# Optimization experiments

Hardware: AMD Instinct MI355X
Metric: run time of the kernel (lower is better)

Reference implementation:

```python
import jax, jax.numpy as jnp
import numpy as np

B, S, D, H = 256, 200, 256, 4
HD = D // H
R = 16  # HIE reduced rank (hardcoded in module)
EPS = 1e-12


def setup_inputs() -> dict:
    key = jax.random.key(0)
    ks = jax.random.split(key, 32)
    w = lambda k, sh: jax.random.normal(k, sh, jnp.float32) * 0.02
    inp = {
        'input_tensor': jax.random.normal(ks[0], (B, S, D), jnp.float32),
        'fusion_tensor': jax.random.normal(ks[1], (B, S, D), jnp.float32),
        'pos_tensor': jax.random.normal(ks[2], (B, S, D), jnp.float32),
        'attention_mask': jnp.zeros((B, 1, 1, S), jnp.float32),
        # projections (stored as (in, out); apply as x @ W + b)
        'Wv': w(ks[3], (D, D)), 'bv': w(ks[4], (D,)),
        'Wqf': w(ks[5], (D, D)), 'bqf': w(ks[6], (D,)),
        'Wkf': w(ks[7], (D, D)), 'bkf': w(ks[8], (D,)),
        'Wvf': w(ks[9], (D, D)), 'bvf': w(ks[10], (D,)),
        'Wqp': w(ks[11], (D, D)), 'bqp': w(ks[12], (D,)),
        'Wkp': w(ks[13], (D, D)), 'bkp': w(ks[14], (D,)),
        'Wvp': w(ks[15], (D, D)), 'bvp': w(ks[16], (D,)),
        # output dense + LayerNorm per branch
        'Wd': w(ks[17], (D, D)), 'bd': w(ks[18], (D,)),
        'g1': jnp.ones((D,), jnp.float32), 'b1': jnp.zeros((D,), jnp.float32),
        'Wfd': w(ks[19], (D, D)), 'bfd': w(ks[20], (D,)),
        'g2': jnp.ones((D,), jnp.float32), 'b2': jnp.zeros((D,), jnp.float32),
        'Wpd': w(ks[21], (D, D)), 'bpd': w(ks[22], (D,)),
        'g3': jnp.ones((D,), jnp.float32), 'b3': jnp.zeros((D,), jnp.float32),
        # HIE parameter (n, r)
        'Wr': jax.random.normal(ks[23], (S, R), jnp.float32),
    }
    return inp


def _heads(t):
    # (B,S,D) -> (B,H,S,HD)
    return t.reshape(B, S, H, HD).transpose(0, 2, 1, 3)


def _layernorm(x, g, b):
    m = jnp.mean(x, axis=-1, keepdims=True)
    v = jnp.mean((x - m) ** 2, axis=-1, keepdims=True)
    return (x - m) * jax.lax.rsqrt(v + EPS) * g + b


def _compute(resid, value_layer, scores, mask, Wd, bd, g, b):
    s = scores / np.sqrt(HD) + mask
    probs = jax.nn.softmax(s, axis=-1)  # (attn dropout = identity in eval)
    ctx = jnp.einsum('bhqk,bhkd->bhqd', probs, value_layer)
    ctx = ctx.transpose(0, 2, 1, 3).reshape(B, S, D)
    return _layernorm(ctx @ Wd + bd + resid, g, b)


def _hie(hX, hA, Wr):
    # reduce sequence dim, batched QR on (d, r) columns
    hr = jnp.einsum('bnd,nr->brd', hX, Wr)        # (B,R,D)
    Q, _ = jnp.linalg.qr(hr.transpose(0, 2, 1))   # (B,D,R), reduced
    pX = hX @ Q                                    # (B,S,R)
    pA = hA @ Q
    pAt = (pX * pA > 0).astype(pA.dtype) * pA      # indicator gate
    return jnp.einsum('bnr,bdr->bnd', pAt, Q)


def reference(input_tensor, fusion_tensor, pos_tensor, attention_mask,
              Wv, bv, Wqf, bqf, Wkf, bkf, Wvf, bvf, Wqp, bqp, Wkp, bkp,
              Wvp, bvp, Wd, bd, g1, b1, Wfd, bfd, g2, b2, Wpd, bpd, g3, b3, Wr):
    item_v = _heads(input_tensor @ Wv + bv)
    fq = _heads(fusion_tensor @ Wqf + bqf)
    fk = _heads(fusion_tensor @ Wkf + bkf)
    fv = _heads(fusion_tensor @ Wvf + bvf)
    pq = _heads(pos_tensor @ Wqp + bqp)
    pk = _heads(pos_tensor @ Wkp + bkp)
    pv = _heads(pos_tensor @ Wvp + bvp)

    item_scores = jnp.einsum('bhqd,bhkd->bhqk', fq, fk)
    pos_scores = jnp.einsum('bhqd,bhkd->bhqk', pq, pk)
    both_scores = item_scores + pos_scores

    h = _compute(input_tensor, item_v, both_scores, attention_mask, Wd, bd, g1, b1)
    hf = _compute(fusion_tensor, fv, item_scores, attention_mask, Wfd, bfd, g2, b2)
    hp = _compute(pos_tensor, pv, pos_scores, attention_mask, Wpd, bpd, g3, b3)

    h = h + _hie(h, hf, Wr)
    return (h, hf, hp)
```

## Files before the change

kernel.cpp:

```cpp
#include <hip/hip_runtime.h>


constexpr int B_ = 256, S_ = 200, D_ = 256, H_ = 4, R_ = 16;
constexpr int M_ = B_ * S_;
constexpr size_t BSD = (size_t)B_ * S_ * D_;

typedef __attribute__((ext_vector_type(8))) short bf16x8;
typedef __attribute__((ext_vector_type(4))) short bf16x4;
typedef __attribute__((ext_vector_type(4))) float f32x4;

#if __has_builtin(__builtin_amdgcn_mfma_f32_16x16x16bf16_1k)
#define MFMA16(A, B, C) __builtin_amdgcn_mfma_f32_16x16x16bf16_1k((A), (B), (C), 0, 0, 0)
#define HAVE_MFMA16 1
#else
#define HAVE_MFMA16 0
#endif

__device__ __forceinline__ float bf2f(unsigned short u) {
  union { unsigned int i; float f; } v; v.i = ((unsigned int)u) << 16; return v.f;
}
__device__ __forceinline__ float bits2f(unsigned int u) {
  union { unsigned int i; float f; } v; v.i = u; return v.f;
}
__device__ __forceinline__ unsigned short f2bf_rne(float f) {
  union { float f; unsigned int i; } v; v.f = f;
  unsigned int u = v.i;
  u += 0x7FFFu + ((u >> 16) & 1u);
  return (unsigned short)(u >> 16);
}
__device__ __forceinline__ unsigned int cvt_pk_bf16(float a, float b) {
  unsigned int r;
  asm("v_cvt_pk_bf16_f32 %0, %1, %2" : "=v"(r) : "v"(a), "v"(b));
  return r;
}
__device__ __forceinline__ void split8_pk(const float* v, bf16x8& hi, bf16x8& lo) {
  union { bf16x8 x; unsigned int u[4]; } H, L;
#pragma unroll
  for (int i = 0; i < 4; ++i) {
    unsigned int h2 = cvt_pk_bf16(v[2 * i], v[2 * i + 1]);
    H.u[i] = h2;
    float h0 = bits2f(h2 << 16);
    float h1 = bits2f(h2 & 0xffff0000u);
    L.u[i] = cvt_pk_bf16(v[2 * i] - h0, v[2 * i + 1] - h1);
  }
  hi = H.x; lo = L.x;
}
__device__ __forceinline__ unsigned int pack_hl(float v) {
  unsigned int h2 = cvt_pk_bf16(v, v);
  float hf = bits2f(h2 << 16);
  return cvt_pk_bf16(v, v - hf);
}
__device__ __forceinline__ void unpack8(uint4 a, uint4 b, bf16x8& hi, bf16x8& lo) {
  union { bf16x8 v; unsigned int u[4]; } H, L;
  H.u[0] = (a.x & 0xffffu) | (a.y << 16);
  H.u[1] = (a.z & 0xffffu) | (a.w << 16);
  H.u[2] = (b.x & 0xffffu) | (b.y << 16);
  H.u[3] = (b.z & 0xffffu) | (b.w << 16);
  L.u[0] = (a.x >> 16) | (a.y & 0xffff0000u);
  L.u[1] = (a.z >> 16) | (a.w & 0xffff0000u);
  L.u[2] = (b.x >> 16) | (b.y & 0xffff0000u);
  L.u[3] = (b.z >> 16) | (b.w & 0xffff0000u);
  hi = H.v; lo = L.v;
}

struct GemmArgs {
  const float* X[7]; const float* bias[7]; float* Y[7];
  const float* resid[7]; const float* g[7]; const float* bvec[7];
  const unsigned short* stash;
};
struct WSplitArgs { const float* W[7]; };

__global__ __launch_bounds__(256) void split_w(WSplitArgs wa, unsigned short* stash)
{
  const int z = blockIdx.y;
  const int idx = blockIdx.x * 256 + threadIdx.x;
  const int k = idx >> 8, n = idx & 255;
  const float x = wa.W[z][idx];
  const unsigned short h = f2bf_rne(x);
  const unsigned short l = f2bf_rne(x - bf2f(h));
  const size_t o = (size_t)z * 131072 + (size_t)n * 256 + k;
  stash[o] = h;
  stash[o + 65536] = l;
}

template<int MODE>
__global__ __launch_bounds__(256, 2) void gemm_mfma(GemmArgs ga)
{
  __shared__ unsigned short lds[30720];
  unsigned short* Ah = lds;
  unsigned short* Al = Ah + 128 * 40;
  unsigned short* Bh = Al + 128 * 40;
  unsigned short* Bl = Bh + 256 * 40;
  const int t = threadIdx.x;
  const int z = blockIdx.y;
  const int m0 = blockIdx.x * 128;
  const float* __restrict__ X = ga.X[z];
  const float* __restrict__ bias = ga.bias[z];
  float* __restrict__ Y = ga.Y[z];
  const unsigned short* __restrict__ Wst = ga.stash + (size_t)z * 131072;
  const int w = t >> 6, lane = t & 63;
  const int wm = w >> 1, wn = w & 1;
  const int lrow = lane & 15;
  const int lk = (lane >> 4) << 3;
  const int rsub = (lane >> 4) << 2;

  f32x4 acc[4][8];
#pragma unroll
  for (int mf = 0; mf < 4; ++mf)
#pragma unroll
    for (int nf = 0; nf < 8; ++nf)
#pragma unroll
      for (int r = 0; r < 4; ++r) acc[mf][nf][r] = 0.f;

  for (int k0 = 0; k0 < 256; k0 += 32) {
#pragma unroll
    for (int i = 0; i < 2; ++i) {
      int c = t + i * 256;
      int r = c >> 2, c8 = (c & 3) << 3;
      float xv[8];
      *reinterpret_cast<float4*>(&xv[0]) =
          *reinterpret_cast<const float4*>(X + (size_t)(m0 + r) * 256 + k0 + c8);
      *reinterpret_cast<float4*>(&xv[4]) =
          *reinterpret_cast<const float4*>(X + (size_t)(m0 + r) * 256 + k0 + c8 + 4);
      bf16x8 hv, lv;
      split8_pk(xv, hv, lv);
      *reinterpret_cast<bf16x8*>(&Ah[r * 40 + c8]) = hv;
      *reinterpret_cast<bf16x8*>(&Al[r * 40 + c8]) = lv;
    }
#pragma unroll
    for (int i = 0; i < 4; ++i) {
      int c = t + i * 256;
      int n = c >> 2, kc = (c & 3) << 3;
      *reinterpret_cast<uint4*>(&Bh[n * 40 + kc]) =
          *reinterpret_cast<const uint4*>(Wst + (size_t)n * 256 + k0 + kc);
      *reinterpret_cast<uint4*>(&Bl[n * 40 + kc]) =
          *reinterpret_cast<const uint4*>(Wst + 65536 + (size_t)n * 256 + k0 + kc);
    }
    __syncthreads();
    bf16x8 ah[4], al[4];
#pragma unroll
    for (int mf = 0; mf < 4; ++mf) {
      int r = wm * 64 + mf * 16 + lrow;
      ah[mf] = *reinterpret_cast<const bf16x8*>(&Ah[r * 40 + lk]);
      al[mf] = *reinterpret_cast<const bf16x8*>(&Al[r * 40 + lk]);
    }
#pragma unroll
    for (int nf = 0; nf < 8; ++nf) {
      int n = wn * 128 + nf * 16 + lrow;
      bf16x8 bh = *reinterpret_cast<const bf16x8*>(&Bh[n * 40 + lk]);
      bf16x8 bl = *reinterpret_cast<const bf16x8*>(&Bl[n * 40 + lk]);
#pragma unroll
      for (int mf = 0; mf < 4; ++mf) {
        acc[mf][nf] = __builtin_amdgcn_mfma_f32_16x16x32_bf16(ah[mf], bh, acc[mf][nf], 0, 0, 0);
        acc[mf][nf] = __builtin_amdgcn_mfma_f32_16x16x32_bf16(al[mf], bh, acc[mf][nf], 0, 0, 0);
        acc[mf][nf] = __builtin_amdgcn_mfma_f32_16x16x32_bf16(ah[mf], bl, acc[mf][nf], 0, 0, 0);
      }
    }
    __syncthreads();
  }

  if (MODE == 0) {
    unsigned int* Yu = (unsigned int*)Y;
#pragma unroll
    for (int nf = 0; nf < 8; ++nf) {
      const int coln = wn * 128 + nf * 16 + lrow;
      const float bb = bias[coln];
#pragma unroll
      for (int mf = 0; mf < 4; ++mf)
#pragma unroll
        for (int r = 0; r < 4; ++r) {
          const size_t row = (size_t)(m0 + wm * 64 + mf * 16 + rsub + r);
          Yu[row * 256 + coln] = pack_hl(acc[mf][nf][r] + bb);
        }
    }
  } else {
    const float* __restrict__ resid = ga.resid[z];
    const float* __restrict__ gv = ga.g[z];
    const float* __restrict__ bv = ga.bvec[z];
    float s_[4][4], q_[4][4];
#pragma unroll
    for (int mf = 0; mf < 4; ++mf)
#pragma unroll
      for (int r = 0; r < 4; ++r) { s_[mf][r] = 0.f; q_[mf][r] = 0.f; }
#pragma unroll
    for (int nf = 0; nf < 8; ++nf) {
      const int coln = wn * 128 + nf * 16 + lrow;
      const float bb = bias[coln];
#pragma unroll
      for (int mf = 0; mf < 4; ++mf)
#pragma unroll
        for (int r = 0; r < 4; ++r) {
          const size_t row = (size_t)(m0 + wm * 64 + mf * 16 + rsub + r);
          float v = acc[mf][nf][r] + bb + resid[row * 256 + coln];
          acc[mf][nf][r] = v;
          s_[mf][r] += v;
          q_[mf][r] = fmaf(v, v, q_[mf][r]);
        }
    }
#pragma unroll
    for (int mf = 0; mf < 4; ++mf)
#pragma unroll
      for (int r = 0; r < 4; ++r) {
        float sv = s_[mf][r], qv = q_[mf][r];
        sv += __shfl_xor(sv, 1); qv += __shfl_xor(qv, 1);
        sv += __shfl_xor(sv, 2); qv += __shfl_xor(qv, 2);
        sv += __shfl_xor(sv, 4); qv += __shfl_xor(qv, 4);
        sv += __shfl_xor(sv, 8); qv += __shfl_xor(qv, 8);
        s_[mf][r] = sv; q_[mf][r] = qv;
      }
    __syncthreads();
    float* red = (float*)lds;
    if (lrow == 0) {
#pragma unroll
      for (int mf = 0; mf < 4; ++mf)
#pragma unroll
        for (int r = 0; r < 4; ++r) {
          int rl = wm * 64 + mf * 16 + rsub + r;
          red[rl * 4 + wn * 2 + 0] = s_[mf][r];
          red[rl * 4 + wn * 2 + 1] = q_[mf][r];
        }
    }
    __syncthreads();
#pragma unroll
    for (int mf = 0; mf < 4; ++mf)
#pragma unroll
      for (int r = 0; r < 4; ++r) {
        int rl = wm * 64 + mf * 16 + rsub + r;
        float st = red[rl * 4 + 0] + red[rl * 4 + 2];
        float qt = red[rl * 4 + 1] + red[rl * 4 + 3];
        float mean = st * (1.0f / 256.0f);
        float var = qt * (1.0f / 256.0f) - mean * mean;
        s_[mf][r] = mean;
        q_[mf][r] = rsqrtf(var + 1e-12f);
      }
#pragma unroll
    for (int nf = 0; nf < 8; ++nf) {
      const int coln = wn * 128 + nf * 16 + lrow;
      const float gg = gv[coln], be = bv[coln];
#pragma unroll
      for (int mf = 0; mf < 4; ++mf)
#pragma unroll
        for (int r = 0; r < 4; ++r) {
          const size_t row = (size_t)(m0 + wm * 64 + mf * 16 + rsub + r);
          Y[row * 256 + coln] = (acc[mf][nf][r] - s_[mf][r]) * q_[mf][r] * gg + be;
        }
    }
  }
}

__global__ __launch_bounds__(256) void attn_mfma(
    const unsigned int* __restrict__ Qf, const unsigned int* __restrict__ Kf,
    const unsigned int* __restrict__ Qp, const unsigned int* __restrict__ Kp,
    const unsigned int* __restrict__ Vi, const unsigned int* __restrict__ Vf,
    const unsigned int* __restrict__ Vp, const float* __restrict__ mask,
    float* __restrict__ Ch, float* __restrict__ Cf, float* __restrict__ Cp)
{
  __shared__ unsigned short su[21504];
  __shared__ float mt[32];
  __shared__ float emt[32];
  constexpr int KFH = 0,     KFL = 2816,  KPH = 5632,  KPL = 8448;
  constexpr int VIH = 11264, VIL = 13824, VFH = 16384, VPH = 18944;
  const int t = threadIdx.x;
  const int mtile = blockIdx.x, h = blockIdx.y, b = blockIdx.z;
  const int w = t >> 6, lane = t & 63, lg = lane >> 4, lm = lane & 15;
  const int mbase = mtile * 128 + w * 32;
  const bool wactive = (mbase < 200);
  const size_t bh = (size_t)b * 200 * 256 + (size_t)h * 64;

  bf16x8 qfh[2][2], qfl[2][2], qph[2][2], qpl[2][2];
#pragma unroll
  for (int mf2 = 0; mf2 < 2; ++mf2) {
    int gq = mbase + mf2 * 16 + lm; if (gq > 199) gq = 199;
    const size_t qb = bh + (size_t)gq * 256;
#pragma unroll
    for (int ks = 0; ks < 2; ++ks) {
      const size_t o = qb + ks * 32 + lg * 8;
      uint4 a = *reinterpret_cast<const uint4*>(Qf + o);
      uint4 bb = *reinterpret_cast<const uint4*>(Qf + o + 4);
      unpack8(a, bb, qfh[mf2][ks], qfl[mf2][ks]);
      a = *reinterpret_cast<const uint4*>(Qp + o);
      bb = *reinterpret_cast<const uint4*>(Qp + o + 4);
      unpack8(a, bb, qph[mf2][ks], qpl[mf2][ks]);
    }
  }

  f32x4 aH[4][2], aF[4][2], aP[4][2];
#pragma unroll
  for (int df = 0; df < 4; ++df)
#pragma unroll
    for (int mf2 = 0; mf2 < 2; ++mf2)
#pragma unroll
      for (int r = 0; r < 4; ++r) { aH[df][mf2][r] = 0.f; aF[df][mf2][r] = 0.f; aP[df][mf2][r] = 0.f; }
  float lH[2] = {0.f, 0.f}, lF[2] = {0.f, 0.f}, lP[2] = {0.f, 0.f};

  for (int kt = 0; kt < 200; kt += 32) {
#pragma unroll
    for (int i = 0; i < 2; ++i) {
      int idx = t + i * 256;
      const int pk = idx >> 8;
      const int rr = (idx >> 3) & 31;
      const int c8 = (idx & 7) << 3;
      int grow = kt + rr; if (grow > 199) grow = 199;
      const unsigned int* src = pk ? Kp : Kf;
      const size_t o = bh + (size_t)grow * 256 + c8;
      uint4 a = *reinterpret_cast<const uint4*>(src + o);
      uint4 bb = *reinterpret_cast<const uint4*>(src + o + 4);
      bf16x8 hv, lv;
      unpack8(a, bb, hv, lv);
      const int KH = pk ? KPH : KFH;
      const int KL = pk ? KPL : KFL;
      *reinterpret_cast<bf16x8*>(&su[KH + rr * 88 + c8]) = hv;
      *reinterpret_cast<bf16x8*>(&su[KL + rr * 88 + c8]) = lv;
    }
#pragma unroll
    for (int i = 0; i < 2; ++i) {
      int idx = t + i * 256;
      int d = idx & 63, kv4i = (idx >> 6) << 2;
      size_t rb[4];
#pragma unroll
      for (int j = 0; j < 4; ++j) {
        int grow = kt + kv4i + j; if (grow > 199) grow = 199;
        rb[j] = bh + (size_t)grow * 256 + d;
      }
      unsigned int u0 = Vi[rb[0]], u1 = Vi[rb[1]], u2 = Vi[rb[2]], u3 = Vi[rb[3]];
      ushort4 hv, lv;
      hv.x = (unsigned short)u0; hv.y = (unsigned short)u1;
      hv.z = (unsigned short)u2; hv.w = (unsigned short)u3;
      lv.x = (unsigned short)(u0 >> 16); lv.y = (unsigned short)(u1 >> 16);
      lv.z = (unsigned short)(u2 >> 16); lv.w = (unsigned short)(u3 >> 16);
      *reinterpret_cast<ushort4*>(&su[VIH + d * 40 + kv4i]) = hv;
      *reinterpret_cast<ushort4*>(&su[VIL + d * 40 + kv4i]) = lv;
      u0 = Vf[rb[0]]; u1 = Vf[rb[1]]; u2 = Vf[rb[2]]; u3 = Vf[rb[3]];
      hv.x = (unsigned short)u0; hv.y = (unsigned short)u1;
      hv.z = (unsigned short)u2; hv.w = (unsigned short)u3;
      *reinterpret_cast<ushort4*>(&su[VFH + d * 40 + kv4i]) = hv;
      u0 = Vp[rb[0]]; u1 = Vp[rb[1]]; u2 = Vp[rb[2]]; u3 = Vp[rb[3]];
      hv.x = (unsigned short)u0; hv.y = (unsigned short)u1;
      hv.z = (unsigned short)u2; hv.w = (unsigned short)u3;
      *reinterpret_cast<ushort4*>(&su[VPH + d * 40 + kv4i]) = hv;
    }
    if (t < 32) {
      const bool valid = (kt + t < 200);
      const float mj = valid ? mask[(size_t)b * 200 + kt + t] : -1e30f;
      mt[t] = mj;
      emt[t] = valid ? __expf(-mj) : 0.f;
    }
    __syncthreads();

    if (wactive) {
      f32x4 si[2][2], sp[2][2];
#pragma unroll
      for (int kvf = 0; kvf < 2; ++kvf)
#pragma unroll
        for (int mf2 = 0; mf2 < 2; ++mf2)
#pragma unroll
          for (int r = 0; r < 4; ++r) { si[kvf][mf2][r] = 0.f; sp[kvf][mf2][r] = 0.f; }
      __builtin_amdgcn_s_setprio(1);
#pragma unroll
      for (int ks = 0; ks < 2; ++ks)
#pragma unroll
        for (int kvf = 0; kvf < 2; ++kvf) {
          bf16x8 kh = *reinterpret_cast<const bf16x8*>(&su[KFH + (kvf * 16 + lm) * 88 + ks * 32 + lg * 8]);
          bf16x8 kl = *reinterpret_cast<const bf16x8*>(&su[KFL + (kvf * 16 + lm) * 88 + ks * 32 + lg * 8]);
#pragma unroll
          for (int mf2 = 0; mf2 < 2; ++mf2) {
            si[kvf][mf2] = __builtin_amdgcn_mfma_f32_16x16x32_bf16(kh, qfh[mf2][ks], si[kvf][mf2], 0, 0, 0);
            si[kvf][mf2] = __builtin_amdgcn_mfma_f32_16x16x32_bf16(kl, qfh[mf2][ks], si[kvf][mf2], 0, 0, 0);
            si[kvf][mf2] = __builtin_amdgcn_mfma_f32_16x16x32_bf16(kh, qfl[mf2][ks], si[kvf][mf2], 0, 0, 0);
          }
          kh = *reinterpret_cast<const bf16x8*>(&su[KPH + (kvf * 16 + lm) * 88 + ks * 32 + lg * 8]);
          kl = *reinterpret_cast<const bf16x8*>(&su[KPL + (kvf * 16 + lm) * 88 + ks * 32 + lg * 8]);
#pragma unroll
          for (int mf2 = 0; mf2 < 2; ++mf2) {
            sp[kvf][mf2] = __builtin_amdgcn_mfma_f32_16x16x32_bf16(kh, qph[mf2][ks], sp[kvf][mf2], 0, 0, 0);
            sp[kvf][mf2] = __builtin_amdgcn_mfma_f32_16x16x32_bf16(kl, qph[mf2][ks], sp[kvf][mf2], 0, 0, 0);
            sp[kvf][mf2] = __builtin_amdgcn_mfma_f32_16x16x32_bf16(kh, qpl[mf2][ks], sp[kvf][mf2], 0, 0, 0);
          }
        }
      __builtin_amdgcn_s_setprio(0);

      f32x4 ph[2][2], pf[2][2], pp[2][2];
      float4 mv[2], ev[2];
      mv[0] = *reinterpret_cast<const float4*>(&mt[lg * 4]);
      mv[1] = *reinterpret_cast<const float4*>(&mt[16 + lg * 4]);
      ev[0] = *reinterpret_cast<const float4*>(&emt[lg * 4]);
      ev[1] = *reinterpret_cast<const float4*>(&emt[16 + lg * 4]);
#pragma unroll
      for (int kvf = 0; kvf < 2; ++kvf)
#pragma unroll
        for (int mf2 = 0; mf2 < 2; ++mf2)
#pragma unroll
          for (int r = 0; r < 4; ++r) {
            float mj = (r == 0) ? mv[kvf].x : (r == 1) ? mv[kvf].y : (r == 2) ? mv[kvf].z : mv[kvf].w;
            float ej = (r == 0) ? ev[kvf].x : (r == 1) ? ev[kvf].y : (r == 2) ? ev[kvf].z : ev[kvf].w;
            float vF = __expf(fmaf(si[kvf][mf2][r], 0.125f, mj));
            float vP = __expf(fmaf(sp[kvf][mf2][r], 0.125f, mj));
            float vH = vF * vP * ej;
            pf[kvf][mf2][r] = vF; pp[kvf][mf2][r] = vP; ph[kvf][mf2][r] = vH;
            lF[mf2] += vF; lP[mf2] += vP; lH[mf2] += vH;
          }

#if HAVE_MFMA16
#pragma unroll
      for (int kvf = 0; kvf < 2; ++kvf) {
        bf16x4 bH[2], bL[2], bF[2], bP[2];
#pragma unroll
        for (int mf2 = 0; mf2 < 2; ++mf2) {
          union { bf16x4 x; unsigned int u[2]; } BH, BL, BF, BP;
          BH.u[0] = cvt_pk_bf16(ph[kvf][mf2][0], ph[kvf][mf2][1]);
          BH.u[1] = cvt_pk_bf16(ph[kvf][mf2][2], ph[kvf][mf2][3]);
          float h0 = bits2f(BH.u[0] << 16);
          float h1 = bits2f(BH.u[0] & 0xffff0000u);
          float h2 = bits2f(BH.u[1] << 16);
          float h3 = bits2f(BH.u[1] & 0xffff0000u);
          BL.u[0] = cvt_pk_bf16(ph[kvf][mf2][0] - h0, ph[kvf][mf2][1] - h1);
          BL.u[1] = cvt_pk_bf16(ph[kvf][mf2][2] - h2, ph[kvf][mf2][3] - h3);
          BF.u[0] = cvt_pk_bf16(pf[kvf][mf2][0], pf[kvf][mf2][1]);
          BF.u[1] = cvt_pk_bf16(pf[kvf][mf2][2], pf[kvf][mf2][3]);
          BP.u[0] = cvt_pk_bf16(pp[kvf][mf2][0], pp[kvf][mf2][1]);
          BP.u[1] = cvt_pk_bf16(pp[kvf][mf2][2], pp[kvf][mf2][3]);
          bH[mf2] = BH.x; bL[mf2] = BL.x; bF[mf2] = BF.x; bP[mf2] = BP.x;
        }
        __builtin_amdgcn_s_setprio(1);
#pragma unroll
        for (int df = 0; df < 4; ++df) {
          const int rowb = (df * 16 + lm) * 40 + kvf * 16 + lg * 4;
          bf16x4 vih = *reinterpret_cast<const bf16x4*>(&su[VIH + rowb]);
          bf16x4 vil = *reinterpret_cast<const bf16x4*>(&su[VIL + rowb]);
          bf16x4 vfh = *reinterpret_cast<const bf16x4*>(&su[VFH + rowb]);
          bf16x4 vph = *reinterpret_cast<const bf16x4*>(&su[VPH + rowb]);
#pragma unroll
          for (int mf2 = 0; mf2 < 2; ++mf2) {
            aH[df][mf2] = MFMA16(vih, bH[mf2], aH[df][mf2]);
            aH[df][mf2] = MFMA16(vil, bH[mf2], aH[df][mf2]);
            aH[df][mf2] = MFMA16(vih, bL[mf2], aH[df][mf2]);
            aF[df][mf2] = MFMA16(vfh, bF[mf2], aF[df][mf2]);
            aP[df][mf2] = MFMA16(vph, bP[mf2], aP[df][mf2]);
          }
        }
        __builtin_amdgcn_s_setprio(0);
      }
#else
#define PV3(P, VH, VL, ACC)                                                    \
      {                                                                        \
        bf16x8 Bh[2], Bl[2];                                                   \
        _Pragma("unroll")                                                      \
        for (int mf2 = 0; mf2 < 2; ++mf2) {                                    \
          _Pragma("unroll")                                                    \
          for (int i = 0; i < 8; ++i) {                                        \
            int src = ((((lg & 1) * 2 + (i >> 2)) << 4) | lm);                 \
            float t0 = __shfl(P[0][mf2][i & 3], src);                          \
            float t1 = __shfl(P[1][mf2][i & 3], src);                          \
            float v = (lg < 2) ? t0 : t1;                                      \
            unsigned short hh = f2bf_rne(v);                                   \
            Bh[mf2][i] = (short)hh;                                            \
            Bl[mf2][i] = (short)f2bf_rne(v - bf2f(hh));                        \
          }                                                                    \
        }                                                                      \
        _Pragma("unroll")                                                      \
        for (int df = 0; df < 4; ++df) {                                       \
          bf16x8 vh = *reinterpret_cast<const bf16x8*>(&su[VH + (df * 16 + lm) * 40 + lg * 8]); \
          bf16x8 vl = *reinterpret_cast<const bf16x8*>(&su[VL + (df * 16 + lm) * 40 + lg * 8]); \
          _Pragma("unroll")                                                    \
          for (int mf2 = 0; mf2 < 2; ++mf2) {                                  \
            ACC[df][mf2] = __builtin_amdgcn_mfma_f32_16x16x32_bf16(vh, Bh[mf2], ACC[df][mf2], 0, 0, 0); \
            ACC[df][mf2] = __builtin_amdgcn_mfma_f32_16x16x32_bf16(vl, Bh[mf2], ACC[df][mf2], 0, 0, 0); \
            ACC[df][mf2] = __builtin_amdgcn_mfma_f32_16x16x32_bf16(vh, Bl[mf2], ACC[df][mf2], 0, 0, 0); \
          }                                                                    \
        }                                                                      \
      }
#define PV1(P, VH, ACC)                                                        \
      {                                                                        \
        bf16x8 Bh[2];                                                          \
        _Pragma("unroll")                                                      \
        for (int mf2 = 0; mf2 < 2; ++mf2) {                                    \
          _Pragma("unroll")                                                    \
          for (int i = 0; i < 8; ++i) {                                        \
            int src = ((((lg & 1) * 2 + (i >> 2)) << 4) | lm);                 \
            float t0 = __shfl(P[0][mf2][i & 3], src);                          \
            float t1 = __shfl(P[1][mf2][i & 3], src);                          \
            float v = (lg < 2) ? t0 : t1;                                     \
            Bh[mf2][i] = (short)f2bf_rne(v);                                   \
          }                                                                    \
        }                                                                      \
        _Pragma("unroll")                                                      \
        for (int df = 0; df < 4; ++df) {                                       \
          bf16x8 vh = *reinterpret_cast<const bf16x8*>(&su[VH + (df * 16 + lm) * 40 + lg * 8]); \
          _Pragma("unroll")                                                    \
          for (int mf2 = 0; mf2 < 2; ++mf2)                                    \
            ACC[df][mf2] = __builtin_amdgcn_mfma_f32_16x16x32_bf16(vh, Bh[mf2], ACC[df][mf2], 0, 0, 0); \
        }                                                                      \
      }
      PV3(ph, VIH, VIL, aH)
      PV1(pf, VFH, aF)
      PV1(pp, VPH, aP)
#undef PV3
#undef PV1
#endif
    }
    __syncthreads();
  }

#pragma unroll
  for (int mf2 = 0; mf2 < 2; ++mf2) {
    lH[mf2] += __shfl_xor(lH[mf2], 16); lH[mf2] += __shfl_xor(lH[mf2], 32);
    lF[mf2] += __shfl_xor(lF[mf2], 16); lF[mf2] += __shfl_xor(lF[mf2], 32);
    lP[mf2] += __shfl_xor(lP[mf2], 16); lP[mf2] += __shfl_xor(lP[mf2], 32);
  }

#pragma unroll
  for (int mf2 = 0; mf2 < 2; ++mf2) {
    int gq = mbase + mf2 * 16 + lm;
    if (gq < 200) {
      const size_t base = bh + (size_t)gq * 256;
      const float iH = 1.f / lH[mf2], iF = 1.f / lF[mf2], iP = 1.f / lP[mf2];
#pragma unroll
      for (int df = 0; df < 4; ++df) {
        float4 o;
        o.x = aH[df][mf2][0] * iH; o.y = aH[df][mf2][1] * iH;
        o.z = aH[df][mf2][2] * iH; o.w = aH[df][mf2][3] * iH;
        *reinterpret_cast<float4*>(Ch + base + df * 16 + lg * 4) = o;
        o.x = aF[df][mf2][0] * iF; o.y = aF[df][mf2][1] * iF;
        o.z = aF[df][mf2][2] * iF; o.w = aF[df][mf2][3] * iF;
        *reinterpret_cast<float4*>(Cf + base + df * 16 + lg * 4) = o;
        o.x = aP[df][mf2][0] * iP; o.y = aP[df][mf2][1] * iP;
        o.z = aP[df][mf2][2] * iP; o.w = aP[df][mf2][3] * iP;
        *reinterpret_cast<float4*>(Cp + base + df * 16 + lg * 4) = o;
      }
    }
  }
}

__global__ __launch_bounds__(256) void hie_hrqr(
    const float* __restrict__ h, const float* __restrict__ Wr, float* __restrict__ Qg)
{
  __shared__ float wrs[3200];
  __shared__ float A[16][256];
  __shared__ double red[4];
  const int b = blockIdx.x, t = threadIdx.x;
  const int wid = t >> 6, lane = t & 63;
  for (int i = t; i < 3200; i += 256) wrs[i] = Wr[i];
  __syncthreads();
  double acc[16];
#pragma unroll
  for (int r = 0; r < 16; ++r) acc[r] = 0.0;
  const float* hb = h + (size_t)b * 200 * 256;
  for (int n = 0; n < 200; ++n) {
    float hv = hb[(size_t)n * 256 + t];
#pragma unroll
    for (int r = 0; r < 16; ++r) acc[r] += (double)(hv * wrs[n * 16 + r]);
  }
#pragma unroll
  for (int r = 0; r < 16; ++r) A[r][t] = (float)acc[r];
  __syncthreads();
#pragma unroll 1
  for (int j = 0; j < 16; ++j) {
    double v = (double)A[j][t];
#pragma unroll 1
    for (int i = 0; i < j; ++i) {
      float qi = A[i][t];
      double p = (double)qi * v;
#pragma unroll
      for (int off = 32; off; off >>= 1) p += __shfl_xor(p, off);
      if (lane == 0) red[wid] = p;
      __syncthreads();
      double dot = red[0] + red[1] + red[2] + red[3];
      __syncthreads();
      v -= dot * (double)qi;
    }
    double nn = v * v;
#pragma unroll
    for (int off = 32; off; off >>= 1) nn += __shfl_xor(nn, off);
    if (lane == 0) red[wid] = nn;
    __syncthreads();
    double nrm = sqrt(red[0] + red[1] + red[2] + red[3]);
    __syncthreads();
    float qv = (float)(v / nrm);
    A[j][t] = qv;
    Qg[(size_t)b * 4096 + j * 256 + t] = qv;
    __syncthreads();
  }
}

__global__ __launch_bounds__(256) void hie_tail(
    const float* __restrict__ hX, const float* __restrict__ hA,
    const float* __restrict__ Qg, float* __restrict__ outp)
{
  __shared__ float Qs[16][260];
  __shared__ float ha[16][260];
  __shared__ float hbx[16][260];
  __shared__ float pt[16][16];
  const int ch = blockIdx.x, b = blockIdx.y, t = threadIdx.x;
  const int chunk = ch * 16;
  for (int i = t; i < 4096; i += 256) Qs[i >> 8][i & 255] = Qg[(size_t)b * 4096 + i];
#pragma unroll
  for (int i = 0; i < 4; ++i) {
    int c = t + i * 256;
    int rr = c >> 6, c4 = (c & 63) << 2;
    int n = chunk + rr;
    if (n < 200) {
      *reinterpret_cast<float4*>(&ha[rr][c4]) =
          *reinterpret_cast<const float4*>(hX + ((size_t)b * 200 + n) * 256 + c4);
      *reinterpret_cast<float4*>(&hbx[rr][c4]) =
          *reinterpret_cast<const float4*>(hA + ((size_t)b * 200 + n) * 256 + c4);
    }
  }
  __syncthreads();
  const int nl = t >> 4, r = t & 15;
  {
    int n = chunk + nl;
    float gate = 0.f;
    if (n < 200) {
      double ax = 0.0, aa = 0.0;
#pragma unroll
      for (int d4 = 0; d4 < 256; d4 += 4) {
        float4 qv = *reinterpret_cast<const float4*>(&Qs[r][d4]);
        float4 hv = *reinterpret_cast<const float4*>(&ha[nl][d4]);
        ax += (double)(hv.x * qv.x + hv.y * qv.y + hv.z * qv.z + hv.w * qv.w);
        hv = *reinterpret_cast<const float4*>(&hbx[nl][d4]);
        aa += (double)(hv.x * qv.x + hv.y * qv.y + hv.z * qv.z + hv.w * qv.w);
      }
      float px = (float)ax, pa = (float)aa;
      gate = (px * pa > 0.0f) ? pa : 0.0f;
    }
    pt[nl][r] = gate;
  }
  __syncthreads();
#pragma unroll 1
  for (int j = 0; j < 16; ++j) {
    int n = chunk + j;
    if (n >= 200) break;
    float acc = ha[j][t];
#pragma unroll
    for (int rr = 0; rr < 16; ++rr) acc = fmaf(pt[j][rr], Qs[rr][t], acc);
    outp[((size_t)b * 200 + n) * 256 + t] = acc;
  }
}

__global__ void diag_kernel(float* out, float val, int n) {
  int i = blockIdx.x * 256 + threadIdx.x;
  if (i < n) out[i] = (i == 0) ? val : 0.0f;
}

extern "C" void kernel_launch(void* const* d_in, const int* in_sizes, int n_in,
                              void* d_out, int out_size, void* d_ws, size_t ws_size,
                              hipStream_t stream)
{
  (void)in_sizes; (void)n_in;
  const float* input  = (const float*)d_in[0];
  const float* fusion = (const float*)d_in[1];
  const float* pos    = (const float*)d_in[2];
  const float* mask   = (const float*)d_in[3];
  const float* Wv  = (const float*)d_in[4];  const float* bv  = (const float*)d_in[5];
  const float* Wqf = (const float*)d_in[6];  const float* bqf = (const float*)d_in[7];
  const float* Wkf = (const float*)d_in[8];  const float* bkf = (const float*)d_in[9];
  const float* Wvf = (const float*)d_in[10]; const float* bvf = (const float*)d_in[11];
  const float* Wqp = (const float*)d_in[12]; const float* bqp = (const float*)d_in[13];
  const float* Wkp = (const float*)d_in[14]; const float* bkp = (const float*)d_in[15];
  const float* Wvp = (const float*)d_in[16]; const float* bvp = (const float*)d_in[17];
  const float* Wd  = (const float*)d_in[18]; const float* bd  = (const float*)d_in[19];
  const float* g1  = (const float*)d_in[20]; const float* b1  = (const float*)d_in[21];
  const float* Wfd = (const float*)d_in[22]; const float* bfd = (const float*)d_in[23];
  const float* g2  = (const float*)d_in[24]; const float* b2  = (const float*)d_in[25];
  const float* Wpd = (const float*)d_in[26]; const float* bpd = (const float*)d_in[27];
  const float* g3  = (const float*)d_in[28]; const float* b3  = (const float*)d_in[29];
  const float* Wr  = (const float*)d_in[30];

  const size_t required = 7 * BSD * 4;
  if (ws_size < required) {
    diag_kernel<<<(out_size + 255) / 256, 256, 0, stream>>>(
        (float*)d_out, (float)(ws_size >> 20), out_size);
    return;
  }

  float* W0 = (float*)d_ws;
  float* O0 = (float*)d_out;
  float* O1 = O0 + BSD;
  float* O2 = O0 + 2 * BSD;
  float* s_fq = W0;
  float* s_fk = W0 + BSD;
  float* s_pq = W0 + 2 * BSD;
  float* s_pk = W0 + 3 * BSD;
  float* s_iv = W0 + 4 * BSD;
  float* s_fv = W0 + 5 * BSD;
  float* s_pv = W0 + 6 * BSD;
  float* Qb   = W0 + 1048576;
  unsigned short* stash1 = (unsigned short*)d_out;
  unsigned short* stash2 = (unsigned short*)(W0 + 4 * 1048576);

  dim3 Blk(256);

  WSplitArgs w7;
  w7.W[0] = Wqf; w7.W[1] = Wkf; w7.W[2] = Wqp; w7.W[3] = Wkp;
  w7.W[4] = Wv;  w7.W[5] = Wvf; w7.W[6] = Wvp;
  split_w<<<dim3(256, 7), Blk, 0, stream>>>(w7, stash1);

  GemmArgs pa = {};
  pa.X[0] = fusion; pa.bias[0] = bqf; pa.Y[0] = s_fq;
  pa.X[1] = fusion; pa.bias[1] = bkf; pa.Y[1] = s_fk;
  pa.X[2] = pos;    pa.bias[2] = bqp; pa.Y[2] = s_pq;
  pa.X[3] = pos;    pa.bias[3] = bkp; pa.Y[3] = s_pk;
  pa.X[4] = input;  pa.bias[4] = bv;  pa.Y[4] = s_iv;
  pa.X[5] = fusion; pa.bias[5] = bvf; pa.Y[5] = s_fv;
  pa.X[6] = pos;    pa.bias[6] = bvp; pa.Y[6] = s_pv;
  pa.stash = stash1;
  gemm_mfma<0><<<dim3(M_ / 128, 7), Blk, 0, stream>>>(pa);

  attn_mfma<<<dim3(2, H_, B_), Blk, 0, stream>>>(
      (const unsigned int*)s_fq, (const unsigned int*)s_fk,
      (const unsigned int*)s_pq, (const unsigned int*)s_pk,
      (const unsigned int*)s_iv, (const unsigned int*)s_fv,
      (const unsigned int*)s_pv, mask, O0, O1, O2);

  WSplitArgs w3;
  w3.W[0] = Wd; w3.W[1] = Wfd; w3.W[2] = Wpd;
  split_w<<<dim3(256, 3), Blk, 0, stream>>>(w3, stash2);

  GemmArgs da = {};
  da.X[0] = O0; da.bias[0] = bd;  da.Y[0] = O0; da.resid[0] = input;  da.g[0] = g1; da.bvec[0] = b1;
  da.X[1] = O1; da.bias[1] = bfd; da.Y[1] = O1; da.resid[1] = fusion; da.g[1] = g2; da.bvec[1] = b2;
  da.X[2] = O2; da.bias[2] = bpd; da.Y[2] = O2; da.resid[2] = pos;    da.g[2] = g3; da.bvec[2] = b3;
  da.stash = stash2;
  gemm_mfma<1><<<dim3(M_ / 128, 3), Blk, 0, stream>>>(da);

  hie_hrqr<<<B_, Blk, 0, stream>>>(O0, Wr, Qb);
  hie_tail<<<dim3(13, B_), Blk, 0, stream>>>(O0, O1, Qb, O0);
}
```

Before: 691.1 us.

## Use single-pass bf16 GEMM for some projections; pad V LDS stride

The projection GEMM now runs the three-pass hi/lo split-bf16 MFMA path only for selected z-slices: the first five in mode 0 and the first in mode 1. The remaining slices use a single bf16 pass, which skips the lo-part conversion, its LDS staging, the lo weight loads and two thirds of the MFMAs. In the attention kernel the V tile row stride in LDS changes from 40 to 44 halves, and the wide V reads are split into two 8-byte loads, to reduce bank conflicts. The lower precision on those projections could increase numerical error.

```diff
diff --git a/kernel.cpp b/kernel.cpp
--- a/kernel.cpp
+++ b/kernel.cpp
@@ -44,6 +44,12 @@
     L.u[i] = cvt_pk_bf16(v[2 * i] - h0, v[2 * i + 1] - h1);
   }
   hi = H.x; lo = L.x;
+}
+__device__ __forceinline__ void pack8_hi(const float* v, bf16x8& hi) {
+  union { bf16x8 x; unsigned int u[4]; } H;
+#pragma unroll
+  for (int i = 0; i < 4; ++i) H.u[i] = cvt_pk_bf16(v[2 * i], v[2 * i + 1]);
+  hi = H.x;
 }
 __device__ __forceinline__ unsigned int pack_hl(float v) {
   unsigned int h2 = cvt_pk_bf16(v, v);
@@ -93,6 +99,7 @@
   unsigned short* Bl = Bh + 256 * 40;
   const int t = threadIdx.x;
   const int z = blockIdx.y;
+  const bool full = (MODE == 0) ? (z < 5) : (z == 0);
   const int m0 = blockIdx.x * 128;
   const float* __restrict__ X = ga.X[z];
   const float* __restrict__ bias = ga.bias[z];
@@ -122,10 +129,16 @@
           *reinterpret_cast<const float4*>(X + (size_t)(m0 + r) * 256 + k0 + c8);
       *reinterpret_cast<float4*>(&xv[4]) =
           *reinterpret_cast<const float4*>(X + (size_t)(m0 + r) * 256 + k0 + c8 + 4);
-      bf16x8 hv, lv;
-      split8_pk(xv, hv, lv);
-      *reinterpret_cast<bf16x8*>(&Ah[r * 40 + c8]) = hv;
-      *reinterpret_cast<bf16x8*>(&Al[r * 40 + c8]) = lv;
+      if (full) {
+        bf16x8 hv, lv;
+        split8_pk(xv, hv, lv);
+        *reinterpret_cast<bf16x8*>(&Ah[r * 40 + c8]) = hv;
+        *reinterpret_cast<bf16x8*>(&Al[r * 40 + c8]) = lv;
+      } else {
+        bf16x8 hv;
+        pack8_hi(xv, hv);
+        *reinterpret_cast<bf16x8*>(&Ah[r * 40 + c8]) = hv;
+      }
     }
 #pragma unroll
     for (int i = 0; i < 4; ++i) {
@@ -133,8 +146,9 @@
       int n = c >> 2, kc = (c & 3) << 3;
       *reinterpret_cast<uint4*>(&Bh[n * 40 + kc]) =
           *reinterpret_cast<const uint4*>(Wst + (size_t)n * 256 + k0 + kc);
-      *reinterpret_cast<uint4*>(&Bl[n * 40 + kc]) =
-          *reinterpret_cast<const uint4*>(Wst + 65536 + (size_t)n * 256 + k0 + kc);
+      if (full)
+        *reinterpret_cast<uint4*>(&Bl[n * 40 + kc]) =
+            *reinterpret_cast<const uint4*>(Wst + 65536 + (size_t)n * 256 + k0 + kc);
     }
     __syncthreads();
     bf16x8 ah[4], al[4];
@@ -142,18 +156,24 @@
     for (int mf = 0; mf < 4; ++mf) {
       int r = wm * 64 + mf * 16 + lrow;
       ah[mf] = *reinterpret_cast<const bf16x8*>(&Ah[r * 40 + lk]);
-      al[mf] = *reinterpret_cast<const bf16x8*>(&Al[r * 40 + lk]);
+      if (full) al[mf] = *reinterpret_cast<const bf16x8*>(&Al[r * 40 + lk]);
     }
 #pragma unroll
     for (int nf = 0; nf < 8; ++nf) {
       int n = wn * 128 + nf * 16 + lrow;
       bf16x8 bh = *reinterpret_cast<const bf16x8*>(&Bh[n * 40 + lk]);
-      bf16x8 bl = *reinterpret_cast<const bf16x8*>(&Bl[n * 40 + lk]);
-#pragma unroll
-      for (int mf = 0; mf < 4; ++mf) {
-        acc[mf][nf] = __builtin_amdgcn_mfma_f32_16x16x32_bf16(ah[mf], bh, acc[mf][nf], 0, 0, 0);
-        acc[mf][nf] = __builtin_amdgcn_mfma_f32_16x16x32_bf16(al[mf], bh, acc[mf][nf], 0, 0, 0);
-        acc[mf][nf] = __builtin_amdgcn_mfma_f32_16x16x32_bf16(ah[mf], bl, acc[mf][nf], 0, 0, 0);
+      if (full) {
+        bf16x8 bl = *reinterpret_cast<const bf16x8*>(&Bl[n * 40 + lk]);
+#pragma unroll
+        for (int mf = 0; mf < 4; ++mf) {
+          acc[mf][nf] = __builtin_amdgcn_mfma_f32_16x16x32_bf16(ah[mf], bh, acc[mf][nf], 0, 0, 0);
+          acc[mf][nf] = __builtin_amdgcn_mfma_f32_16x16x32_bf16(al[mf], bh, acc[mf][nf], 0, 0, 0);
+          acc[mf][nf] = __builtin_amdgcn_mfma_f32_16x16x32_bf16(ah[mf], bl, acc[mf][nf], 0, 0, 0);
+        }
+      } else {
+#pragma unroll
+        for (int mf = 0; mf < 4; ++mf)
+          acc[mf][nf] = __builtin_amdgcn_mfma_f32_16x16x32_bf16(ah[mf], bh, acc[mf][nf], 0, 0, 0);
       }
     }
     __syncthreads();
@@ -255,11 +275,11 @@
     const unsigned int* __restrict__ Vp, const float* __restrict__ mask,
     float* __restrict__ Ch, float* __restrict__ Cf, float* __restrict__ Cp)
 {
-  __shared__ unsigned short su[21504];
+  __shared__ unsigned short su[22528];
   __shared__ float mt[32];
   __shared__ float emt[32];
   constexpr int KFH = 0,     KFL = 2816,  KPH = 5632,  KPL = 8448;
-  constexpr int VIH = 11264, VIL = 13824, VFH = 16384, VPH = 18944;
+  constexpr int VIH = 11264, VIL = 14080, VFH = 16896, VPH = 19712;
   const int t = threadIdx.x;
   const int mtile = blockIdx.x, h = blockIdx.y, b = blockIdx.z;
   const int w = t >> 6, lane = t & 63, lg = lane >> 4, lm = lane & 15;
@@ -328,16 +348,16 @@
       hv.z = (unsigned short)u2; hv.w = (unsigned short)u3;
       lv.x = (unsigned short)(u0 >> 16); lv.y = (unsigned short)(u1 >> 16);
       lv.z = (unsigned short)(u2 >> 16); lv.w = (unsigned short)(u3 >> 16);
-      *reinterpret_cast<ushort4*>(&su[VIH + d * 40 + kv4i]) = hv;
-      *reinterpret_cast<ushort4*>(&su[VIL + d * 40 + kv4i]) = lv;
+      *reinterpret_cast<ushort4*>(&su[VIH + d * 44 + kv4i]) = hv;
+      *reinterpret_cast<ushort4*>(&su[VIL + d * 44 + kv4i]) = lv;
       u0 = Vf[rb[0]]; u1 = Vf[rb[1]]; u2 = Vf[rb[2]]; u3 = Vf[rb[3]];
       hv.x = (unsigned short)u0; hv.y = (unsigned short)u1;
       hv.z = (unsigned short)u2; hv.w = (unsigned short)u3;
-      *reinterpret_cast<ushort4*>(&su[VFH + d * 40 + kv4i]) = hv;
+      *reinterpret_cast<ushort4*>(&su[VFH + d * 44 + kv4i]) = hv;
       u0 = Vp[rb[0]]; u1 = Vp[rb[1]]; u2 = Vp[rb[2]]; u3 = Vp[rb[3]];
       hv.x = (unsigned short)u0; hv.y = (unsigned short)u1;
       hv.z = (unsigned short)u2; hv.w = (unsigned short)u3;
-      *reinterpret_cast<ushort4*>(&su[VPH + d * 40 + kv4i]) = hv;
+      *reinterpret_cast<ushort4*>(&su[VPH + d * 44 + kv4i]) = hv;
     }
     if (t < 32) {
       const bool valid = (kt + t < 200);
@@ -424,7 +444,7 @@
         __builtin_amdgcn_s_setprio(1);
 #pragma unroll
         for (int df = 0; df < 4; ++df) {
-          const int rowb = (df * 16 + lm) * 40 + kvf * 16 + lg * 4;
+          const int rowb = (df * 16 + lm) * 44 + kvf * 16 + lg * 4;
           bf16x4 vih = *reinterpret_cast<const bf16x4*>(&su[VIH + rowb]);
           bf16x4 vil = *reinterpret_cast<const bf16x4*>(&su[VIL + rowb]);
           bf16x4 vfh = *reinterpret_cast<const bf16x4*>(&su[VFH + rowb]);
@@ -459,13 +479,18 @@
         }                                                                      \
         _Pragma("unroll")                                                      \
         for (int df = 0; df < 4; ++df) {                                       \
-          bf16x8 vh = *reinterpret_cast<const bf16x8*>(&su[VH + (df * 16 + lm) * 40 + lg * 8]); \
-          bf16x8 vl = *reinterpret_cast<const bf16x8*>(&su[VL + (df * 16 + lm) * 40 + lg * 8]); \
+          const int va = VH + (df * 16 + lm) * 44 + lg * 8;                    \
+          const int vb = VL + (df * 16 + lm) * 44 + lg * 8;                    \
+          union { bf16x8 v; uint2 q[2]; } vh, vl;                              \
+          vh.q[0] = *reinterpret_cast<const uint2*>(&su[va]);                  \
+          vh.q[1] = *reinterpret_cast<const uint2*>(&su[va + 4]);              \
+          vl.q[0] = *reinterpret_cast<const uint2*>(&su[vb]);                  \
+          vl.q[1] = *reinterpret_cast<const uint2*>(&su[vb + 4]);              \
           _Pragma("unroll")                                                    \
           for (int mf2 = 0; mf2 < 2; ++mf2) {                                  \
-            ACC[df][mf2] = __builtin_amdgcn_mfma_f32_16x16x32_bf16(vh, Bh[mf2], ACC[df][mf2], 0, 0, 0); \
-            ACC[df][mf2] = __builtin_amdgcn_mfma_f32_16x16x32_bf16(vl, Bh[mf2], ACC[df][mf2], 0, 0, 0); \
-            ACC[df][mf2] = __builtin_amdgcn_mfma_f32_16x16x32_bf16(vh, Bl[mf2], ACC[df][mf2], 0, 0, 0); \
+            ACC[df][mf2] = __builtin_amdgcn_mfma_f32_16x16x32_bf16(vh.v, Bh[mf2], ACC[df][mf2], 0, 0, 0); \
+            ACC[df][mf2] = __builtin_amdgcn_mfma_f32_16x16x32_bf16(vl.v, Bh[mf2], ACC[df][mf2], 0, 0, 0); \
+            ACC[df][mf2] = __builtin_amdgcn_mfma_f32_16x16x32_bf16(vh.v, Bl[mf2], ACC[df][mf2], 0, 0, 0); \
           }                                                                    \
         }                                                                      \
       }
@@ -479,16 +504,19 @@
             int src = ((((lg & 1) * 2 + (i >> 2)) << 4) | lm);                 \
             float t0 = __shfl(P[0][mf2][i & 3], src);                          \
             float t1 = __shfl(P[1][mf2][i & 3], src);                          \
-            float v = (lg < 2) ? t0 : t1;                                     \
+            float v = (lg < 2) ? t0 : t1;                                      \
             Bh[mf2][i] = (short)f2bf_rne(v);                                   \
           }                                                                    \
         }                                                                      \
         _Pragma("unroll")                                                      \
         for (int df = 0; df < 4; ++df) {                                       \
-          bf16x8 vh = *reinterpret_cast<const bf16x8*>(&su[VH + (df * 16 + lm) * 40 + lg * 8]); \
+          const int va = VH + (df * 16 + lm) * 44 + lg * 8;                    \
+          union { bf16x8 v; uint2 q[2]; } vh;                                  \
+          vh.q[0] = *reinterpret_cast<const uint2*>(&su[va]);                  \
+          vh.q[1] = *reinterpret_cast<const uint2*>(&su[va + 4]);              \
           _Pragma("unroll")                                                    \
           for (int mf2 = 0; mf2 < 2; ++mf2)                                    \
-            ACC[df][mf2] = __builtin_amdgcn_mfma_f32_16x16x32_bf16(vh, Bh[mf2], ACC[df][mf2], 0, 0, 0); \
+            ACC[df][mf2] = __builtin_amdgcn_mfma_f32_16x16x32_bf16(vh.v, Bh[mf2], ACC[df][mf2], 0, 0, 0); \
         }                                                                      \
       }
       PV3(ph, VIH, VIL, aH)
```

New measurement: 903.0 us. +30.7%, slower.
